# Kernel tuning notes

Measured on AMD Instinct MI355X. Metric: run time of the kernel, lower is better.

Reference implementation:

```python
import jax, jax.numpy as jnp
import numpy as np

B, T, D, H = 8, 1024, 1024, 16
HS = D // H
EPS = 1e-5


def setup_inputs() -> dict:
    key = jax.random.key(0)
    ks = jax.random.split(key, 8)
    w = lambda k, sh: (jax.random.normal(k, sh, jnp.float32) * 0.02)
    return {
        "x": jax.random.normal(ks[0], (B, T, D), jnp.float32),
        "Wq": w(ks[1], (D, D)),
        "Wk": w(ks[2], (D, D)),
        "Wv": w(ks[3], (D, D)),
        "Wo": w(ks[4], (D, D)),
        "bo": jnp.zeros((D,), jnp.float32),
        "W1": w(ks[5], (D, 4 * D)),
        "b1": jnp.zeros((4 * D,), jnp.float32),
        "W2": w(ks[6], (4 * D, D)),
        "b2": jnp.zeros((D,), jnp.float32),
        "ln1_g": jnp.ones((D,), jnp.float32),
        "ln1_b": jnp.zeros((D,), jnp.float32),
        "ln2_g": jnp.ones((D,), jnp.float32),
        "ln2_b": jnp.zeros((D,), jnp.float32),
    }


def _ln(y, g, b):
    m = y.mean(-1, keepdims=True)
    v = ((y - m) ** 2).mean(-1, keepdims=True)
    return (y - m) * jax.lax.rsqrt(v + EPS) * g + b


def reference(x, Wq, Wk, Wv, Wo, bo, W1, b1, W2, b2, ln1_g, ln1_b, ln2_g, ln2_b):
    Bx, Tx, Dx = x.shape
    h = _ln(x, ln1_g, ln1_b)
    # per-head projections (heads concatenated along columns of Wq/Wk/Wv)
    q = (h @ Wq).reshape(Bx, Tx, H, HS).transpose(0, 2, 1, 3)  # [B,H,T,hs]
    k = (h @ Wk).reshape(Bx, Tx, H, HS).transpose(0, 2, 1, 3)
    v = (h @ Wv).reshape(Bx, Tx, H, HS).transpose(0, 2, 1, 3)
    # NOTE: original scales by 1/sqrt(C) with C = d_model, not head_size
    wei = jnp.einsum("bhqd,bhkd->bhqk", q, k) / jnp.sqrt(jnp.float32(Dx))
    mask = jnp.tril(jnp.ones((Tx, Tx), bool))
    wei = jnp.where(mask, wei, -jnp.inf)
    wei = jax.nn.softmax(wei, axis=-1)
    att = jnp.einsum("bhqk,bhkd->bhqd", wei, v)
    att = att.transpose(0, 2, 1, 3).reshape(Bx, Tx, Dx)  # concat heads
    x = x + att @ Wo + bo
    h2 = _ln(x, ln2_g, ln2_b)
    x = x + jax.nn.relu(h2 @ W1 + b1) @ W2 + b2
    return x
```

## Files before the change

### kernel.cpp

```cpp
#include <hip/hip_runtime.h>
#include <stdint.h>
#include <stddef.h>

typedef unsigned short u16;
typedef u16 u16x4 __attribute__((ext_vector_type(4)));
typedef u16 u16x8 __attribute__((ext_vector_type(8)));
typedef __bf16 bf16x8 __attribute__((ext_vector_type(8)));
typedef float f32x4 __attribute__((ext_vector_type(4)));

__device__ __forceinline__ float b2f(u16 u) {
    return __uint_as_float(((unsigned)u) << 16);
}
__device__ __forceinline__ u16 f2b(float f) {
    unsigned u = __float_as_uint(f);
    u += 0x7FFF + ((u >> 16) & 1);
    return (u16)(u >> 16);
}
__device__ __forceinline__ bf16x8 bcast(u16x8 v) { return __builtin_bit_cast(bf16x8, v); }
__device__ __forceinline__ f32x4 mfma16(bf16x8 a, bf16x8 b, f32x4 c) {
    return __builtin_amdgcn_mfma_f32_16x16x32_bf16(a, b, c, 0, 0, 0);
}
typedef const __attribute__((address_space(1))) void* gas1;
typedef __attribute__((address_space(3))) void* las3;
__device__ __forceinline__ void gload_lds16(const void* g, void* l) {
    __builtin_amdgcn_global_load_lds((gas1)g, (las3)l, 16, 0, 0);
}

#define DPP_ROR_F32(x, N) __builtin_bit_cast(float, __builtin_amdgcn_update_dpp( \
    __builtin_bit_cast(int, (x)), __builtin_bit_cast(int, (x)), 0x120 + (N), 0xf, 0xf, false))
__device__ __forceinline__ float red_max16(float x) {
    x = fmaxf(x, DPP_ROR_F32(x, 8));
    x = fmaxf(x, DPP_ROR_F32(x, 4));
    x = fmaxf(x, DPP_ROR_F32(x, 2));
    x = fmaxf(x, DPP_ROR_F32(x, 1));
    return x;
}
__device__ __forceinline__ float red_add16(float x) {
    x += DPP_ROR_F32(x, 8);
    x += DPP_ROR_F32(x, 4);
    x += DPP_ROR_F32(x, 2);
    x += DPP_ROR_F32(x, 1);
    return x;
}

__global__ __launch_bounds__(256) void transpose_k(const float* __restrict__ in,
                                                   u16* __restrict__ out,
                                                   int R, int C) {
    __shared__ u16 t[32][33];
    int x = blockIdx.x * 32 + threadIdx.x;
    int y0 = blockIdx.y * 32;
#pragma unroll
    for (int j = threadIdx.y; j < 32; j += 8)
        t[j][threadIdx.x] = f2b(in[(size_t)(y0 + j) * C + x]);
    __syncthreads();
    int xo = y0 + threadIdx.x;
    int yo0 = blockIdx.x * 32;
#pragma unroll
    for (int j = threadIdx.y; j < 32; j += 8)
        out[(size_t)(yo0 + j) * R + xo] = t[threadIdx.x][j];
}

__global__ __launch_bounds__(256) void ln_k(const void* __restrict__ x,
                                            const float* __restrict__ g,
                                            const float* __restrict__ b,
                                            u16* __restrict__ y,
                                            int x_f32) {
    const int row = blockIdx.x;
    const size_t ro = (size_t)row * 1024;
    float v[4], s = 0.0f, ss = 0.0f;
#pragma unroll
    for (int i = 0; i < 4; ++i) {
        size_t idx = ro + threadIdx.x + i * 256;
        float f = x_f32 ? ((const float*)x)[idx] : b2f(((const u16*)x)[idx]);
        v[i] = f; s += f; ss += f * f;
    }
#pragma unroll
    for (int off = 32; off; off >>= 1) {
        s += __shfl_down(s, off);
        ss += __shfl_down(ss, off);
    }
    __shared__ float red[2][4];
    int wave = threadIdx.x >> 6, lane = threadIdx.x & 63;
    if (lane == 0) { red[0][wave] = s; red[1][wave] = ss; }
    __syncthreads();
    s = red[0][0] + red[0][1] + red[0][2] + red[0][3];
    ss = red[1][0] + red[1][1] + red[1][2] + red[1][3];
    float mean = s * (1.0f / 1024.0f);
    float var = ss * (1.0f / 1024.0f) - mean * mean;
    float inv = rsqrtf(var + 1e-5f);
#pragma unroll
    for (int i = 0; i < 4; ++i) {
        int c = threadIdx.x + i * 256;
        float o = (v[i] - mean) * inv * g[c] + b[c];
        y[ro + c] = f2b(o);
    }
}

__device__ __forceinline__ void gemm128_core(const u16* __restrict__ A,
                                             const u16* __restrict__ Bt,
                                             const int Ksz, const int m0,
                                             const int n0, u16* lds,
                                             f32x4 (&acc)[4][2]) {
    char* ldsb = (char*)lds;
    const int tid = threadIdx.x;
    const int w = tid >> 6, lane = tid & 63;
    const int quad = lane >> 4, l16 = lane & 15;
    const int wr = w >> 2, wc = w & 3;
    const int rS = w * 8 + (lane >> 3);
    const int cS = ((lane & 7) ^ (lane >> 3)) * 8;
    const int dstW = w * 1024;
    const int xo = (l16 & 7) << 4;
    const int co0 = (quad * 16) ^ xo;
    const int co1 = (64 + quad * 16) ^ xo;
    const int aoffB = wr * 8192 + l16 * 128;
    const int boffB = wc * 4096 + l16 * 128;
    const u16* pA = A + (size_t)(m0 + rS) * Ksz + cS;
    const u16* pB = Bt + (size_t)(n0 + rS) * Ksz + cS;
    const int nK = Ksz >> 6;
    const size_t rstep = (size_t)64 * Ksz;

#define STG_A(dd, kt) do { \
    const u16* _s = pA + (size_t)(kt) * 64; \
    char* _d = ldsb + (dd) * 16384 + dstW; \
    gload_lds16(_s, _d); \
    gload_lds16(_s + rstep, _d + 8192); \
} while (0)
#define STG_B(dd, kt) do { \
    const u16* _s = pB + (size_t)(kt) * 64; \
    char* _d = ldsb + 32768 + (dd) * 16384 + dstW; \
    gload_lds16(_s, _d); \
    gload_lds16(_s + rstep, _d + 8192); \
} while (0)

    bf16x8 af[2][4], bg[2][2];

#define LDA128() do { \
    _Pragma("unroll") for (int mi = 0; mi < 4; ++mi) { \
        af[0][mi] = bcast(*(const u16x8*)(ldsA + mi * 2048 + co0)); \
        af[1][mi] = bcast(*(const u16x8*)(ldsA + mi * 2048 + co1)); \
    } \
} while (0)
#define LDB128(n2) do { \
    bg[0][n2] = bcast(*(const u16x8*)(ldsBp + (n2) * 2048 + co0)); \
    bg[1][n2] = bcast(*(const u16x8*)(ldsBp + (n2) * 2048 + co1)); \
} while (0)
#define QUAD128(n2) do { \
    _Pragma("unroll") for (int mi = 0; mi < 4; ++mi) { \
        acc[mi][n2] = mfma16(af[0][mi], bg[0][n2], acc[mi][n2]); \
        acc[mi][n2] = mfma16(af[1][mi], bg[1][n2], acc[mi][n2]); \
    } \
} while (0)

    STG_A(0, 0); STG_B(0, 0);
    asm volatile("s_waitcnt vmcnt(0)" ::: "memory");
    __builtin_amdgcn_s_barrier();
    asm volatile("" ::: "memory");

    for (int t = 0; t < nK; ++t) {
        const int d = t & 1, e = d ^ 1;
        const char* ldsA = ldsb + d * 16384 + aoffB;
        const char* ldsBp = ldsb + 32768 + d * 16384 + boffB;
        if (t + 1 < nK) { STG_A(e, t + 1); STG_B(e, t + 1); }
        LDA128(); LDB128(0);
        asm volatile("s_waitcnt lgkmcnt(0)" ::: "memory");
        __builtin_amdgcn_s_setprio(1);
        QUAD128(0);
        __builtin_amdgcn_s_setprio(0);
        LDB128(1);
        asm volatile("s_waitcnt lgkmcnt(0)" ::: "memory");
        __builtin_amdgcn_s_setprio(1);
        QUAD128(1);
        __builtin_amdgcn_s_setprio(0);
        asm volatile("s_waitcnt vmcnt(0)" ::: "memory");
        __builtin_amdgcn_s_barrier();
        asm volatile("" ::: "memory");
    }
#undef STG_A
#undef STG_B
#undef LDA128
#undef LDB128
#undef QUAD128
}

__global__ __launch_bounds__(512, 4) void gemm128(const u16* __restrict__ A,
                                                  const u16* __restrict__ Bt,
                                                  void* __restrict__ Cout,
                                                  int M, int N, int K,
                                                  const float* __restrict__ bias,
                                                  const void* __restrict__ resid,
                                                  int relu, int resid_f32, int out_f32) {
    (void)M;
    __shared__ __attribute__((aligned(16))) u16 lds[32768];
    f32x4 acc[4][2] = {};
    const int m0 = blockIdx.y * 128, n0 = blockIdx.x * 128;
    gemm128_core(A, Bt, K, m0, n0, lds, acc);
    const int tid = threadIdx.x;
    const int w = tid >> 6, lane = tid & 63;
    const int quad = lane >> 4, l16 = lane & 15;
    const int wr = w >> 2, wc = w & 3;
    if (out_f32) {
#pragma unroll
        for (int n2 = 0; n2 < 2; ++n2) {
            const int col = n0 + wc * 32 + n2 * 16 + l16;
            const float bv = bias ? bias[col] : 0.0f;
#pragma unroll
            for (int mi = 0; mi < 4; ++mi) {
#pragma unroll
                for (int r = 0; r < 4; ++r) {
                    const size_t idx = (size_t)(m0 + wr * 64 + mi * 16 + quad * 4 + r) * N + col;
                    float val = acc[mi][n2][r] + bv;
                    if (resid)
                        val += resid_f32 ? ((const float*)resid)[idx]
                                         : b2f(((const u16*)resid)[idx]);
                    if (relu) val = fmaxf(val, 0.0f);
                    ((float*)Cout)[idx] = val;
                }
            }
        }
    } else {
#pragma unroll
        for (int n2 = 0; n2 < 2; ++n2) {
            const int dcol = wc * 32 + n2 * 16 + l16;
            const int col = n0 + dcol;
            const float bv = bias ? bias[col] : 0.0f;
#pragma unroll
            for (int mi = 0; mi < 4; ++mi) {
#pragma unroll
                for (int r = 0; r < 4; ++r) {
                    const int lr = wr * 64 + mi * 16 + quad * 4 + r;
                    float val = acc[mi][n2][r] + bv;
                    if (resid) {
                        const size_t idx = (size_t)(m0 + lr) * N + col;
                        val += resid_f32 ? ((const float*)resid)[idx]
                                         : b2f(((const u16*)resid)[idx]);
                    }
                    if (relu) val = fmaxf(val, 0.0f);
                    lds[lr * 136 + dcol] = f2b(val);
                }
            }
        }
        __syncthreads();
        const int sr = tid >> 4, sc = (tid & 15) * 8;
        u16* gout = (u16*)Cout + (size_t)m0 * N + n0;
#pragma unroll
        for (int p = 0; p < 4; ++p) {
            const int rr = p * 32 + sr;
            u16x8 v = *(const u16x8*)&lds[rr * 136 + sc];
            *(u16x8*)&gout[(size_t)rr * N + sc] = v;
        }
    }
}

__global__ __launch_bounds__(512, 4) void gemm128_qkv(const u16* __restrict__ A,
                                                      const u16* __restrict__ Bt,
                                                      u16* __restrict__ qb,
                                                      u16* __restrict__ kb,
                                                      u16* __restrict__ vbT) {
    __shared__ __attribute__((aligned(16))) u16 lds[32768];
    f32x4 acc[4][2] = {};
    const int m0 = blockIdx.y * 128, n0 = blockIdx.x * 128;
    gemm128_core(A, Bt, 1024, m0, n0, lds, acc);
    const int tid = threadIdx.x;
    const int w = tid >> 6, lane = tid & 63;
    const int quad = lane >> 4, l16 = lane & 15;
    const int wr = w >> 2, wc = w & 3;
    const int tens = blockIdx.x >> 3;
    const int nbase = (blockIdx.x & 7) * 128;
    const int sr = tid >> 4, sc = (tid & 15) * 8;
    if (tens < 2) {
        u16* dst = tens ? kb : qb;
#pragma unroll
        for (int n2 = 0; n2 < 2; ++n2) {
            const int dcol = wc * 32 + n2 * 16 + l16;
#pragma unroll
            for (int mi = 0; mi < 4; ++mi)
#pragma unroll
                for (int r = 0; r < 4; ++r)
                    lds[(wr * 64 + mi * 16 + quad * 4 + r) * 136 + dcol] =
                        f2b(acc[mi][n2][r]);
        }
        __syncthreads();
        u16* gout = dst + (size_t)m0 * 1024 + nbase;
#pragma unroll
        for (int p = 0; p < 4; ++p) {
            const int rr = p * 32 + sr;
            u16x8 v = *(const u16x8*)&lds[rr * 136 + sc];
            *(u16x8*)&gout[(size_t)rr * 1024 + sc] = v;
        }
    } else {
#pragma unroll
        for (int n2 = 0; n2 < 2; ++n2) {
            const int dcol = wc * 32 + n2 * 16 + l16;
#pragma unroll
            for (int mi = 0; mi < 4; ++mi)
#pragma unroll
                for (int r = 0; r < 4; ++r)
                    lds[dcol * 136 + wr * 64 + mi * 16 + quad * 4 + r] =
                        f2b(acc[mi][n2][r]);
        }
        __syncthreads();
        const int b = m0 >> 10, t0 = m0 & 1023;
#pragma unroll
        for (int p = 0; p < 4; ++p) {
            const int dd = p * 32 + sr;
            const int h = (nbase + dd) >> 6, d6 = (nbase + dd) & 63;
            u16x8 v = *(const u16x8*)&lds[dd * 136 + sc];
            *(u16x8*)&vbT[(((size_t)(b * 16 + h) * 64 + d6) << 10) + t0 + sc] = v;
        }
    }
}

__global__ __launch_bounds__(256) void attn_k(const u16* __restrict__ q,
                                              const u16* __restrict__ k,
                                              const u16* __restrict__ vt,
                                              u16* __restrict__ att) {
    __shared__ __attribute__((aligned(16))) u16 Ks[64][72];
    __shared__ __attribute__((aligned(16))) u16 Vts[64][72];
    __shared__ __attribute__((aligned(16))) u16 QP[128 * 72];
    const int bh = blockIdx.y;
    const int bb = bh >> 4, hd = bh & 15;
    const size_t base  = (size_t)bb * 1024 * 1024 + (size_t)hd * 64;
    const size_t vbase = (size_t)bh << 16;
    const int tid = threadIdx.x;
    const int w = tid >> 6, lane = tid & 63;
    const int quad = lane >> 4, l16 = lane & 15;
    u16* Ps = &QP[(w * 32) * 72];

    for (int half = 0; half < 2; ++half) {
        const int qt = half ? blockIdx.x : 7 - blockIdx.x;
        const int q0 = qt * 128;
        __syncthreads();

#pragma unroll
        for (int it = 0; it < 4; ++it) {
            int f = it * 256 + tid;
            int r = f >> 3, c8 = (f & 7) * 8;
            *(u16x8*)&QP[r * 72 + c8] = *(const u16x8*)(q + base + (size_t)(q0 + r) * 1024 + c8);
        }
        __syncthreads();
        bf16x8 qf[2][2];
#pragma unroll
        for (int qi = 0; qi < 2; ++qi)
#pragma unroll
            for (int ks = 0; ks < 2; ++ks)
                qf[qi][ks] = bcast(*(const u16x8*)&QP[(w * 32 + qi * 16 + l16) * 72 + ks * 32 + quad * 8]);

        f32x4 oacc[2][4] = {};
        float mrow[2][4], lrow[2][4];
#pragma unroll
        for (int qi = 0; qi < 2; ++qi)
#pragma unroll
            for (int r = 0; r < 4; ++r) { mrow[qi][r] = -1e30f; lrow[qi][r] = 0.0f; }

        const int njt = qt * 2 + 2;
        for (int jt = 0; jt < njt; ++jt) {
            const int j0 = jt * 64;
#pragma unroll
            for (int it = 0; it < 2; ++it) {
                int f = it * 256 + tid;
                int r = f >> 3, c8 = (f & 7) * 8;
                *(u16x8*)&Ks[r][c8]  = *(const u16x8*)(k  + base  + (size_t)(j0 + r) * 1024 + c8);
                *(u16x8*)&Vts[r][c8] = *(const u16x8*)(vt + vbase + (size_t)r * 1024 + j0 + c8);
            }
            __syncthreads();

            f32x4 s[2][4] = {};
#pragma unroll
            for (int kj = 0; kj < 4; ++kj) {
                bf16x8 b0 = bcast(*(const u16x8*)&Ks[kj * 16 + l16][quad * 8]);
                bf16x8 b1 = bcast(*(const u16x8*)&Ks[kj * 16 + l16][32 + quad * 8]);
#pragma unroll
                for (int qi = 0; qi < 2; ++qi) {
                    s[qi][kj] = mfma16(qf[qi][0], b0, s[qi][kj]);
                    s[qi][kj] = mfma16(qf[qi][1], b1, s[qi][kj]);
                }
            }

            float tmax[2][4], alpha[2][4], rs[2][4];
            if (jt >= 2 * qt) {
#pragma unroll
                for (int qi = 0; qi < 2; ++qi)
#pragma unroll
                    for (int r = 0; r < 4; ++r) {
                        const int qrow = q0 + w * 32 + qi * 16 + quad * 4 + r;
                        float tm = -1e30f;
#pragma unroll
                        for (int kj = 0; kj < 4; ++kj) {
                            const int col = j0 + kj * 16 + l16;
                            float sv = s[qi][kj][r] * 0.03125f;
                            sv = (col > qrow) ? -1e30f : sv;
                            s[qi][kj][r] = sv;
                            tm = fmaxf(tm, sv);
                        }
                        tmax[qi][r] = tm;
                    }
            } else {
#pragma unroll
                for (int qi = 0; qi < 2; ++qi)
#pragma unroll
                    for (int r = 0; r < 4; ++r) {
                        float tm = -1e30f;
#pragma unroll
                        for (int kj = 0; kj < 4; ++kj) {
                            float sv = s[qi][kj][r] * 0.03125f;
                            s[qi][kj][r] = sv;
                            tm = fmaxf(tm, sv);
                        }
                        tmax[qi][r] = tm;
                    }
            }
#pragma unroll
            for (int qi = 0; qi < 2; ++qi)
#pragma unroll
                for (int r = 0; r < 4; ++r)
                    tmax[qi][r] = red_max16(tmax[qi][r]);
            int grow = 0;
#pragma unroll
            for (int qi = 0; qi < 2; ++qi)
#pragma unroll
                for (int r = 0; r < 4; ++r)
                    grow |= (tmax[qi][r] > mrow[qi][r]) ? 1 : 0;
            const bool rescale = __any(grow);
            if (rescale) {
#pragma unroll
                for (int qi = 0; qi < 2; ++qi)
#pragma unroll
                    for (int r = 0; r < 4; ++r) {
                        float mnew = fmaxf(mrow[qi][r], tmax[qi][r]);
                        alpha[qi][r] = __expf(mrow[qi][r] - mnew);
                        mrow[qi][r] = mnew;
                    }
            }
#pragma unroll
            for (int qi = 0; qi < 2; ++qi)
#pragma unroll
                for (int r = 0; r < 4; ++r) {
                    const float m = mrow[qi][r];
                    float accp = 0.0f;
#pragma unroll
                    for (int kj = 0; kj < 4; ++kj) {
                        float p = __expf(s[qi][kj][r] - m);
                        s[qi][kj][r] = p;
                        accp += p;
                    }
                    rs[qi][r] = accp;
                }
#pragma unroll
            for (int qi = 0; qi < 2; ++qi)
#pragma unroll
                for (int r = 0; r < 4; ++r)
                    rs[qi][r] = red_add16(rs[qi][r]);
            if (rescale) {
#pragma unroll
                for (int qi = 0; qi < 2; ++qi)
#pragma unroll
                    for (int r = 0; r < 4; ++r) {
                        lrow[qi][r] = lrow[qi][r] * alpha[qi][r] + rs[qi][r];
#pragma unroll
                        for (int oj = 0; oj < 4; ++oj) oacc[qi][oj][r] *= alpha[qi][r];
                    }
            } else {
#pragma unroll
                for (int qi = 0; qi < 2; ++qi)
#pragma unroll
                    for (int r = 0; r < 4; ++r)
                        lrow[qi][r] += rs[qi][r];
            }
#pragma unroll
            for (int qi = 0; qi < 2; ++qi)
#pragma unroll
                for (int r = 0; r < 4; ++r)
#pragma unroll
                    for (int kj = 0; kj < 4; ++kj)
                        Ps[(qi * 16 + quad * 4 + r) * 72 + kj * 16 + l16] = f2b(s[qi][kj][r]);

#pragma unroll
            for (int ks = 0; ks < 2; ++ks) {
                bf16x8 a0 = bcast(*(const u16x8*)&Ps[(l16) * 72 + ks * 32 + quad * 8]);
                bf16x8 a1 = bcast(*(const u16x8*)&Ps[(16 + l16) * 72 + ks * 32 + quad * 8]);
#pragma unroll
                for (int oj = 0; oj < 4; ++oj) {
                    bf16x8 bv = bcast(*(const u16x8*)&Vts[oj * 16 + l16][ks * 32 + quad * 8]);
                    oacc[0][oj] = mfma16(a0, bv, oacc[0][oj]);
                    oacc[1][oj] = mfma16(a1, bv, oacc[1][oj]);
                }
            }
            __syncthreads();
        }
#pragma unroll
        for (int qi = 0; qi < 2; ++qi)
#pragma unroll
            for (int oj = 0; oj < 4; ++oj)
#pragma unroll
                for (int r = 0; r < 4; ++r) {
                    int row = q0 + w * 32 + qi * 16 + quad * 4 + r;
                    float o = oacc[qi][oj][r] / lrow[qi][r];
                    att[base + (size_t)row * 1024 + oj * 16 + l16] = f2b(o);
                }
    }
}

extern "C" void kernel_launch(void* const* d_in, const int* in_sizes, int n_in,
                              void* d_out, int out_size, void* d_ws, size_t ws_size,
                              hipStream_t stream) {
    (void)in_sizes; (void)n_in; (void)out_size;
    const float* x   = (const float*)d_in[0];
    const float* Wq  = (const float*)d_in[1];
    const float* Wk  = (const float*)d_in[2];
    const float* Wv  = (const float*)d_in[3];
    const float* Wo  = (const float*)d_in[4];
    const float* bo  = (const float*)d_in[5];
    const float* W1  = (const float*)d_in[6];
    const float* b1  = (const float*)d_in[7];
    const float* W2  = (const float*)d_in[8];
    const float* b2  = (const float*)d_in[9];
    const float* g1  = (const float*)d_in[10];
    const float* be1 = (const float*)d_in[11];
    const float* g2  = (const float*)d_in[12];
    const float* be2 = (const float*)d_in[13];
    float* out = (float*)d_out;

    u16* ws = (u16*)d_ws;
    const size_t MIO = 1024u * 1024u;
    u16* Wt0 = ws;
    u16* Wt1 = ws + 4 * MIO;
    u16* qb  = ws + 8 * MIO;
    u16* kb  = ws + 16 * MIO;
    u16* vb  = ws + 24 * MIO;
    u16* mid = ws + 32 * MIO;
    u16* hb  = (u16*)d_out;
    const int full_ffn = ws_size >= (size_t)64 * MIO * 2;

    dim3 tb32(32, 8);

    ln_k<<<8192, 256, 0, stream>>>(x, g1, be1, hb, 1);

    transpose_k<<<dim3(32, 32), tb32, 0, stream>>>(Wq, Wt0,           1024, 1024);
    transpose_k<<<dim3(32, 32), tb32, 0, stream>>>(Wk, Wt0 + 1 * MIO, 1024, 1024);
    transpose_k<<<dim3(32, 32), tb32, 0, stream>>>(Wv, Wt0 + 2 * MIO, 1024, 1024);
    gemm128_qkv<<<dim3(24, 64), 512, 0, stream>>>(hb, Wt0, qb, kb, vb);

    attn_k<<<dim3(4, 128), 256, 0, stream>>>(qb, kb, vb, hb);

    transpose_k<<<dim3(32, 32), tb32, 0, stream>>>(Wo, Wt1, 1024, 1024);
    gemm128<<<dim3(8, 64), 512, 0, stream>>>(hb, Wt1, qb, 8192, 1024, 1024, bo, x, 0, 1, 0);

    ln_k<<<8192, 256, 0, stream>>>(qb, g2, be2, kb, 0);

    transpose_k<<<dim3(128, 32), tb32, 0, stream>>>(W1, Wt0, 1024, 4096);
    transpose_k<<<dim3(32, 128), tb32, 0, stream>>>(W2, Wt1, 4096, 1024);
    if (full_ffn) {
        gemm128<<<dim3(32, 64), 512, 0, stream>>>(kb, Wt0, mid, 8192, 4096, 1024, b1, nullptr, 1, 0, 0);
        gemm128<<<dim3(8, 64), 512, 0, stream>>>(mid, Wt1, out, 8192, 1024, 4096, b2, qb, 0, 0, 1);
    } else {
        for (int c = 0; c < 4; ++c) {
            const size_t ro = (size_t)c * 2048 * 1024;
            gemm128<<<dim3(32, 16), 512, 0, stream>>>(kb + ro, Wt0, vb, 2048, 4096, 1024, b1, nullptr, 1, 0, 0);
            gemm128<<<dim3(8, 16), 512, 0, stream>>>(vb, Wt1, out + ro, 2048, 1024, 4096, b2, qb + ro, 0, 0, 1);
        }
    }
}
```

Measured before the change: 486.8 us.

## Switch 128x128 GEMM blocks to 4 waves with 64x64 per-wave tiles

Reorganizes the GEMM blocks from 8 waves (each computing 64x32) to 4 waves (each computing 64x64). Each wave now loads more B fragments per K-step and issues 32 MFMAs per fragment load instead of two half-batches, which raises register reuse and cuts LDS reads per flop. Staging uses four 16-byte async loads per thread per operand, and the epilogues write 8 row-chunks. The trade-offs are fewer waves per block, higher register pressure from the 4x4 accumulators, and less latency hiding within each block.

```diff
diff --git a/kernel.cpp b/kernel.cpp
--- a/kernel.cpp
+++ b/kernel.cpp
@@ -100,12 +100,12 @@
                                              const u16* __restrict__ Bt,
                                              const int Ksz, const int m0,
                                              const int n0, u16* lds,
-                                             f32x4 (&acc)[4][2]) {
+                                             f32x4 (&acc)[4][4]) {
     char* ldsb = (char*)lds;
     const int tid = threadIdx.x;
     const int w = tid >> 6, lane = tid & 63;
     const int quad = lane >> 4, l16 = lane & 15;
-    const int wr = w >> 2, wc = w & 3;
+    const int wr = w >> 1, wc = w & 1;
     const int rS = w * 8 + (lane >> 3);
     const int cS = ((lane & 7) ^ (lane >> 3)) * 8;
     const int dstW = w * 1024;
@@ -113,41 +113,46 @@
     const int co0 = (quad * 16) ^ xo;
     const int co1 = (64 + quad * 16) ^ xo;
     const int aoffB = wr * 8192 + l16 * 128;
-    const int boffB = wc * 4096 + l16 * 128;
+    const int boffB = wc * 8192 + l16 * 128;
     const u16* pA = A + (size_t)(m0 + rS) * Ksz + cS;
     const u16* pB = Bt + (size_t)(n0 + rS) * Ksz + cS;
     const int nK = Ksz >> 6;
-    const size_t rstep = (size_t)64 * Ksz;
+    const size_t r32 = (size_t)32 * Ksz;
 
 #define STG_A(dd, kt) do { \
     const u16* _s = pA + (size_t)(kt) * 64; \
     char* _d = ldsb + (dd) * 16384 + dstW; \
     gload_lds16(_s, _d); \
-    gload_lds16(_s + rstep, _d + 8192); \
+    gload_lds16(_s + r32, _d + 4096); \
+    gload_lds16(_s + 2 * r32, _d + 8192); \
+    gload_lds16(_s + 3 * r32, _d + 12288); \
 } while (0)
 #define STG_B(dd, kt) do { \
     const u16* _s = pB + (size_t)(kt) * 64; \
     char* _d = ldsb + 32768 + (dd) * 16384 + dstW; \
     gload_lds16(_s, _d); \
-    gload_lds16(_s + rstep, _d + 8192); \
+    gload_lds16(_s + r32, _d + 4096); \
+    gload_lds16(_s + 2 * r32, _d + 8192); \
+    gload_lds16(_s + 3 * r32, _d + 12288); \
 } while (0)
 
-    bf16x8 af[2][4], bg[2][2];
-
-#define LDA128() do { \
+    bf16x8 af[2][4], bg[2][4];
+
+#define LDAB() do { \
     _Pragma("unroll") for (int mi = 0; mi < 4; ++mi) { \
         af[0][mi] = bcast(*(const u16x8*)(ldsA + mi * 2048 + co0)); \
         af[1][mi] = bcast(*(const u16x8*)(ldsA + mi * 2048 + co1)); \
     } \
+    _Pragma("unroll") for (int nj = 0; nj < 4; ++nj) { \
+        bg[0][nj] = bcast(*(const u16x8*)(ldsBp + nj * 2048 + co0)); \
+        bg[1][nj] = bcast(*(const u16x8*)(ldsBp + nj * 2048 + co1)); \
+    } \
 } while (0)
-#define LDB128(n2) do { \
-    bg[0][n2] = bcast(*(const u16x8*)(ldsBp + (n2) * 2048 + co0)); \
-    bg[1][n2] = bcast(*(const u16x8*)(ldsBp + (n2) * 2048 + co1)); \
-} while (0)
-#define QUAD128(n2) do { \
-    _Pragma("unroll") for (int mi = 0; mi < 4; ++mi) { \
-        acc[mi][n2] = mfma16(af[0][mi], bg[0][n2], acc[mi][n2]); \
-        acc[mi][n2] = mfma16(af[1][mi], bg[1][n2], acc[mi][n2]); \
+#define QUADALL() do { \
+    _Pragma("unroll") for (int mi = 0; mi < 4; ++mi) \
+    _Pragma("unroll") for (int nj = 0; nj < 4; ++nj) { \
+        acc[mi][nj] = mfma16(af[0][mi], bg[0][nj], acc[mi][nj]); \
+        acc[mi][nj] = mfma16(af[1][mi], bg[1][nj], acc[mi][nj]); \
     } \
 } while (0)
 
@@ -161,15 +166,10 @@
         const char* ldsA = ldsb + d * 16384 + aoffB;
         const char* ldsBp = ldsb + 32768 + d * 16384 + boffB;
         if (t + 1 < nK) { STG_A(e, t + 1); STG_B(e, t + 1); }
-        LDA128(); LDB128(0);
+        LDAB();
         asm volatile("s_waitcnt lgkmcnt(0)" ::: "memory");
         __builtin_amdgcn_s_setprio(1);
-        QUAD128(0);
-        __builtin_amdgcn_s_setprio(0);
-        LDB128(1);
-        asm volatile("s_waitcnt lgkmcnt(0)" ::: "memory");
-        __builtin_amdgcn_s_setprio(1);
-        QUAD128(1);
+        QUADALL();
         __builtin_amdgcn_s_setprio(0);
         asm volatile("s_waitcnt vmcnt(0)" ::: "memory");
         __builtin_amdgcn_s_barrier();
@@ -177,12 +177,11 @@
     }
 #undef STG_A
 #undef STG_B
-#undef LDA128
-#undef LDB128
-#undef QUAD128
-}
-
-__global__ __launch_bounds__(512, 4) void gemm128(const u16* __restrict__ A,
+#undef LDAB
+#undef QUADALL
+}
+
+__global__ __launch_bounds__(256, 2) void gemm128(const u16* __restrict__ A,
                                                   const u16* __restrict__ Bt,
                                                   void* __restrict__ Cout,
                                                   int M, int N, int K,
@@ -191,24 +190,24 @@
                                                   int relu, int resid_f32, int out_f32) {
     (void)M;
     __shared__ __attribute__((aligned(16))) u16 lds[32768];
-    f32x4 acc[4][2] = {};
+    f32x4 acc[4][4] = {};
     const int m0 = blockIdx.y * 128, n0 = blockIdx.x * 128;
     gemm128_core(A, Bt, K, m0, n0, lds, acc);
     const int tid = threadIdx.x;
     const int w = tid >> 6, lane = tid & 63;
     const int quad = lane >> 4, l16 = lane & 15;
-    const int wr = w >> 2, wc = w & 3;
+    const int wr = w >> 1, wc = w & 1;
     if (out_f32) {
 #pragma unroll
-        for (int n2 = 0; n2 < 2; ++n2) {
-            const int col = n0 + wc * 32 + n2 * 16 + l16;
+        for (int nj = 0; nj < 4; ++nj) {
+            const int col = n0 + wc * 64 + nj * 16 + l16;
             const float bv = bias ? bias[col] : 0.0f;
 #pragma unroll
             for (int mi = 0; mi < 4; ++mi) {
 #pragma unroll
                 for (int r = 0; r < 4; ++r) {
                     const size_t idx = (size_t)(m0 + wr * 64 + mi * 16 + quad * 4 + r) * N + col;
-                    float val = acc[mi][n2][r] + bv;
+                    float val = acc[mi][nj][r] + bv;
                     if (resid)
                         val += resid_f32 ? ((const float*)resid)[idx]
                                          : b2f(((const u16*)resid)[idx]);
@@ -219,8 +218,8 @@
         }
     } else {
 #pragma unroll
-        for (int n2 = 0; n2 < 2; ++n2) {
-            const int dcol = wc * 32 + n2 * 16 + l16;
+        for (int nj = 0; nj < 4; ++nj) {
+            const int dcol = wc * 64 + nj * 16 + l16;
             const int col = n0 + dcol;
             const float bv = bias ? bias[col] : 0.0f;
 #pragma unroll
@@ -228,7 +227,7 @@
 #pragma unroll
                 for (int r = 0; r < 4; ++r) {
                     const int lr = wr * 64 + mi * 16 + quad * 4 + r;
-                    float val = acc[mi][n2][r] + bv;
+                    float val = acc[mi][nj][r] + bv;
                     if (resid) {
                         const size_t idx = (size_t)(m0 + lr) * N + col;
                         val += resid_f32 ? ((const float*)resid)[idx]
@@ -243,66 +242,66 @@
         const int sr = tid >> 4, sc = (tid & 15) * 8;
         u16* gout = (u16*)Cout + (size_t)m0 * N + n0;
 #pragma unroll
-        for (int p = 0; p < 4; ++p) {
-            const int rr = p * 32 + sr;
+        for (int p = 0; p < 8; ++p) {
+            const int rr = p * 16 + sr;
             u16x8 v = *(const u16x8*)&lds[rr * 136 + sc];
             *(u16x8*)&gout[(size_t)rr * N + sc] = v;
         }
     }
 }
 
-__global__ __launch_bounds__(512, 4) void gemm128_qkv(const u16* __restrict__ A,
+__global__ __launch_bounds__(256, 2) void gemm128_qkv(const u16* __restrict__ A,
                                                       const u16* __restrict__ Bt,
                                                       u16* __restrict__ qb,
                                                       u16* __restrict__ kb,
                                                       u16* __restrict__ vbT) {
     __shared__ __attribute__((aligned(16))) u16 lds[32768];
-    f32x4 acc[4][2] = {};
+    f32x4 acc[4][4] = {};
     const int m0 = blockIdx.y * 128, n0 = blockIdx.x * 128;
     gemm128_core(A, Bt, 1024, m0, n0, lds, acc);
     const int tid = threadIdx.x;
     const int w = tid >> 6, lane = tid & 63;
     const int quad = lane >> 4, l16 = lane & 15;
-    const int wr = w >> 2, wc = w & 3;
+    const int wr = w >> 1, wc = w & 1;
     const int tens = blockIdx.x >> 3;
     const int nbase = (blockIdx.x & 7) * 128;
     const int sr = tid >> 4, sc = (tid & 15) * 8;
     if (tens < 2) {
         u16* dst = tens ? kb : qb;
 #pragma unroll
-        for (int n2 = 0; n2 < 2; ++n2) {
-            const int dcol = wc * 32 + n2 * 16 + l16;
+        for (int nj = 0; nj < 4; ++nj) {
+            const int dcol = wc * 64 + nj * 16 + l16;
 #pragma unroll
             for (int mi = 0; mi < 4; ++mi)
 #pragma unroll
                 for (int r = 0; r < 4; ++r)
                     lds[(wr * 64 + mi * 16 + quad * 4 + r) * 136 + dcol] =
-                        f2b(acc[mi][n2][r]);
+                        f2b(acc[mi][nj][r]);
         }
         __syncthreads();
         u16* gout = dst + (size_t)m0 * 1024 + nbase;
 #pragma unroll
-        for (int p = 0; p < 4; ++p) {
-            const int rr = p * 32 + sr;
+        for (int p = 0; p < 8; ++p) {
+            const int rr = p * 16 + sr;
             u16x8 v = *(const u16x8*)&lds[rr * 136 + sc];
             *(u16x8*)&gout[(size_t)rr * 1024 + sc] = v;
         }
     } else {
 #pragma unroll
-        for (int n2 = 0; n2 < 2; ++n2) {
-            const int dcol = wc * 32 + n2 * 16 + l16;
+        for (int nj = 0; nj < 4; ++nj) {
+            const int dcol = wc * 64 + nj * 16 + l16;
 #pragma unroll
             for (int mi = 0; mi < 4; ++mi)
 #pragma unroll
                 for (int r = 0; r < 4; ++r)
                     lds[dcol * 136 + wr * 64 + mi * 16 + quad * 4 + r] =
-                        f2b(acc[mi][n2][r]);
+                        f2b(acc[mi][nj][r]);
         }
         __syncthreads();
         const int b = m0 >> 10, t0 = m0 & 1023;
 #pragma unroll
-        for (int p = 0; p < 4; ++p) {
-            const int dd = p * 32 + sr;
+        for (int p = 0; p < 8; ++p) {
+            const int dd = p * 16 + sr;
             const int h = (nbase + dd) >> 6, d6 = (nbase + dd) & 63;
             u16x8 v = *(const u16x8*)&lds[dd * 136 + sc];
             *(u16x8*)&vbT[(((size_t)(b * 16 + h) * 64 + d6) << 10) + t0 + sc] = v;
@@ -538,25 +537,25 @@
     transpose_k<<<dim3(32, 32), tb32, 0, stream>>>(Wq, Wt0,           1024, 1024);
     transpose_k<<<dim3(32, 32), tb32, 0, stream>>>(Wk, Wt0 + 1 * MIO, 1024, 1024);
     transpose_k<<<dim3(32, 32), tb32, 0, stream>>>(Wv, Wt0 + 2 * MIO, 1024, 1024);
-    gemm128_qkv<<<dim3(24, 64), 512, 0, stream>>>(hb, Wt0, qb, kb, vb);
+    gemm128_qkv<<<dim3(24, 64), 256, 0, stream>>>(hb, Wt0, qb, kb, vb);
 
     attn_k<<<dim3(4, 128), 256, 0, stream>>>(qb, kb, vb, hb);
 
     transpose_k<<<dim3(32, 32), tb32, 0, stream>>>(Wo, Wt1, 1024, 1024);
-    gemm128<<<dim3(8, 64), 512, 0, stream>>>(hb, Wt1, qb, 8192, 1024, 1024, bo, x, 0, 1, 0);
+    gemm128<<<dim3(8, 64), 256, 0, stream>>>(hb, Wt1, qb, 8192, 1024, 1024, bo, x, 0, 1, 0);
 
     ln_k<<<8192, 256, 0, stream>>>(qb, g2, be2, kb, 0);
 
     transpose_k<<<dim3(128, 32), tb32, 0, stream>>>(W1, Wt0, 1024, 4096);
     transpose_k<<<dim3(32, 128), tb32, 0, stream>>>(W2, Wt1, 4096, 1024);
     if (full_ffn) {
-        gemm128<<<dim3(32, 64), 512, 0, stream>>>(kb, Wt0, mid, 8192, 4096, 1024, b1, nullptr, 1, 0, 0);
-        gemm128<<<dim3(8, 64), 512, 0, stream>>>(mid, Wt1, out, 8192, 1024, 4096, b2, qb, 0, 0, 1);
+        gemm128<<<dim3(32, 64), 256, 0, stream>>>(kb, Wt0, mid, 8192, 4096, 1024, b1, nullptr, 1, 0, 0);
+        gemm128<<<dim3(8, 64), 256, 0, stream>>>(mid, Wt1, out, 8192, 1024, 4096, b2, qb, 0, 0, 1);
     } else {
         for (int c = 0; c < 4; ++c) {
             const size_t ro = (size_t)c * 2048 * 1024;
-            gemm128<<<dim3(32, 16), 512, 0, stream>>>(kb + ro, Wt0, vb, 2048, 4096, 1024, b1, nullptr, 1, 0, 0);
-            gemm128<<<dim3(8, 16), 512, 0, stream>>>(vb, Wt1, out + ro, 2048, 1024, 4096, b2, qb + ro, 0, 0, 1);
-        }
-    }
-}
+            gemm128<<<dim3(32, 16), 256, 0, stream>>>(kb + ro, Wt0, vb, 2048, 4096, 1024, b1, nullptr, 1, 0, 0);
+            gemm128<<<dim3(8, 16), 256, 0, stream>>>(vb, Wt1, out + ro, 2048, 1024, 4096, b2, qb + ro, 0, 0, 1);
+        }
+    }
+}
```

Result: slower. 517.8 us (+6.4%).

## Halve GEMM K-tile to 32 and raise occupancy to eight blocks per CU

Applied to the files above, without the earlier changes.

The shared 128x128 GEMM core now stages K-tiles of 32 instead of 64, with one 16-byte global-to-LDS load per thread per operand and a new XOR swizzle and fragment layout. LDS drops from 64KB to about 34KB per block, and launch bounds rise from 4 to 8 blocks per CU, aiming to hide latency through occupancy. The cost is twice as many K-iterations and barriers, with fewer MFMAs between them, and tighter register budgets under the higher occupancy hint.

```diff
diff --git a/kernel.cpp b/kernel.cpp
--- a/kernel.cpp
+++ b/kernel.cpp
@@ -106,83 +106,59 @@
     const int w = tid >> 6, lane = tid & 63;
     const int quad = lane >> 4, l16 = lane & 15;
     const int wr = w >> 2, wc = w & 3;
-    const int rS = w * 8 + (lane >> 3);
-    const int cS = ((lane & 7) ^ (lane >> 3)) * 8;
-    const int dstW = w * 1024;
-    const int xo = (l16 & 7) << 4;
-    const int co0 = (quad * 16) ^ xo;
-    const int co1 = (64 + quad * 16) ^ xo;
-    const int aoffB = wr * 8192 + l16 * 128;
-    const int boffB = wc * 4096 + l16 * 128;
+    const int rS = tid >> 2;
+    const int cS = ((tid & 3) ^ (rS & 3)) * 8;
+    const int co = l16 * 64 + ((quad ^ (l16 & 3)) << 4);
+    const int aoff = wr * 4096;
+    const int boff = wc * 2048;
     const u16* pA = A + (size_t)(m0 + rS) * Ksz + cS;
     const u16* pB = Bt + (size_t)(n0 + rS) * Ksz + cS;
-    const int nK = Ksz >> 6;
-    const size_t rstep = (size_t)64 * Ksz;
-
-#define STG_A(dd, kt) do { \
-    const u16* _s = pA + (size_t)(kt) * 64; \
-    char* _d = ldsb + (dd) * 16384 + dstW; \
-    gload_lds16(_s, _d); \
-    gload_lds16(_s + rstep, _d + 8192); \
+    const int nK = Ksz >> 5;
+
+#define STG(dd, kt) do { \
+    gload_lds16(pA + (size_t)(kt) * 32, ldsb + (dd) * 8192 + tid * 16); \
+    gload_lds16(pB + (size_t)(kt) * 32, ldsb + 16384 + (dd) * 8192 + tid * 16); \
 } while (0)
-#define STG_B(dd, kt) do { \
-    const u16* _s = pB + (size_t)(kt) * 64; \
-    char* _d = ldsb + 32768 + (dd) * 16384 + dstW; \
-    gload_lds16(_s, _d); \
-    gload_lds16(_s + rstep, _d + 8192); \
+
+    bf16x8 af[4], bg[2];
+
+#define LDAB() do { \
+    _Pragma("unroll") for (int mi = 0; mi < 4; ++mi) \
+        af[mi] = bcast(*(const u16x8*)(ldsA + mi * 1024 + co)); \
+    _Pragma("unroll") for (int n2 = 0; n2 < 2; ++n2) \
+        bg[n2] = bcast(*(const u16x8*)(ldsBp + n2 * 1024 + co)); \
 } while (0)
-
-    bf16x8 af[2][4], bg[2][2];
-
-#define LDA128() do { \
-    _Pragma("unroll") for (int mi = 0; mi < 4; ++mi) { \
-        af[0][mi] = bcast(*(const u16x8*)(ldsA + mi * 2048 + co0)); \
-        af[1][mi] = bcast(*(const u16x8*)(ldsA + mi * 2048 + co1)); \
-    } \
+#define QUADALL() do { \
+    _Pragma("unroll") for (int mi = 0; mi < 4; ++mi) \
+    _Pragma("unroll") for (int n2 = 0; n2 < 2; ++n2) \
+        acc[mi][n2] = mfma16(af[mi], bg[n2], acc[mi][n2]); \
 } while (0)
-#define LDB128(n2) do { \
-    bg[0][n2] = bcast(*(const u16x8*)(ldsBp + (n2) * 2048 + co0)); \
-    bg[1][n2] = bcast(*(const u16x8*)(ldsBp + (n2) * 2048 + co1)); \
-} while (0)
-#define QUAD128(n2) do { \
-    _Pragma("unroll") for (int mi = 0; mi < 4; ++mi) { \
-        acc[mi][n2] = mfma16(af[0][mi], bg[0][n2], acc[mi][n2]); \
-        acc[mi][n2] = mfma16(af[1][mi], bg[1][n2], acc[mi][n2]); \
-    } \
-} while (0)
-
-    STG_A(0, 0); STG_B(0, 0);
+
+    STG(0, 0);
     asm volatile("s_waitcnt vmcnt(0)" ::: "memory");
     __builtin_amdgcn_s_barrier();
     asm volatile("" ::: "memory");
 
     for (int t = 0; t < nK; ++t) {
         const int d = t & 1, e = d ^ 1;
-        const char* ldsA = ldsb + d * 16384 + aoffB;
-        const char* ldsBp = ldsb + 32768 + d * 16384 + boffB;
-        if (t + 1 < nK) { STG_A(e, t + 1); STG_B(e, t + 1); }
-        LDA128(); LDB128(0);
+        const char* ldsA = ldsb + d * 8192 + aoff;
+        const char* ldsBp = ldsb + 16384 + d * 8192 + boff;
+        if (t + 1 < nK) STG(e, t + 1);
+        LDAB();
         asm volatile("s_waitcnt lgkmcnt(0)" ::: "memory");
         __builtin_amdgcn_s_setprio(1);
-        QUAD128(0);
-        __builtin_amdgcn_s_setprio(0);
-        LDB128(1);
-        asm volatile("s_waitcnt lgkmcnt(0)" ::: "memory");
-        __builtin_amdgcn_s_setprio(1);
-        QUAD128(1);
+        QUADALL();
         __builtin_amdgcn_s_setprio(0);
         asm volatile("s_waitcnt vmcnt(0)" ::: "memory");
         __builtin_amdgcn_s_barrier();
         asm volatile("" ::: "memory");
     }
-#undef STG_A
-#undef STG_B
-#undef LDA128
-#undef LDB128
-#undef QUAD128
-}
-
-__global__ __launch_bounds__(512, 4) void gemm128(const u16* __restrict__ A,
+#undef STG
+#undef LDAB
+#undef QUADALL
+}
+
+__global__ __launch_bounds__(512, 8) void gemm128(const u16* __restrict__ A,
                                                   const u16* __restrict__ Bt,
                                                   void* __restrict__ Cout,
                                                   int M, int N, int K,
@@ -190,7 +166,7 @@
                                                   const void* __restrict__ resid,
                                                   int relu, int resid_f32, int out_f32) {
     (void)M;
-    __shared__ __attribute__((aligned(16))) u16 lds[32768];
+    __shared__ __attribute__((aligned(16))) u16 lds[17408];
     f32x4 acc[4][2] = {};
     const int m0 = blockIdx.y * 128, n0 = blockIdx.x * 128;
     gemm128_core(A, Bt, K, m0, n0, lds, acc);
@@ -251,12 +227,12 @@
     }
 }
 
-__global__ __launch_bounds__(512, 4) void gemm128_qkv(const u16* __restrict__ A,
+__global__ __launch_bounds__(512, 8) void gemm128_qkv(const u16* __restrict__ A,
                                                       const u16* __restrict__ Bt,
                                                       u16* __restrict__ qb,
                                                       u16* __restrict__ kb,
                                                       u16* __restrict__ vbT) {
-    __shared__ __attribute__((aligned(16))) u16 lds[32768];
+    __shared__ __attribute__((aligned(16))) u16 lds[17408];
     f32x4 acc[4][2] = {};
     const int m0 = blockIdx.y * 128, n0 = blockIdx.x * 128;
     gemm128_core(A, Bt, 1024, m0, n0, lds, acc);
```

After: 532.9 us. 9.5% more time.
